# Performance work log

Hardware: AMD Instinct MI355X
Metric: run time of the kernel (lower is better)

The kernel has to match this reference:

```python
import jax, jax.numpy as jnp
import numpy as np

C = 1024
H = 16
D = C // H

def setup_inputs() -> dict:
    key = jax.random.key(0)
    ks = jax.random.split(key, 12)
    s = 1.0 / np.sqrt(C)
    inp = {
        "Q": jax.random.normal(ks[0], (2, 1024, C), jnp.float32),
        "K_in": jax.random.normal(ks[1], (2, 4096, C), jnp.float32),
        "V_in": jax.random.normal(ks[2], (2, 4096, C), jnp.float32),
        "V_bias": jax.random.normal(ks[3], (2, 4096), jnp.float32),
        "Wq_w": jax.random.uniform(ks[4], (C, C), jnp.float32, -s, s),
        "Wq_b": jax.random.uniform(ks[5], (C,), jnp.float32, -s, s),
        "Wk_w": jax.random.uniform(ks[6], (C, C), jnp.float32, -s, s),
        "Wk_b": jax.random.uniform(ks[7], (C,), jnp.float32, -s, s),
        "Wv_w": jax.random.uniform(ks[8], (C, C), jnp.float32, -s, s),
        "Wv_b": jax.random.uniform(ks[9], (C,), jnp.float32, -s, s),
        "Wo_w": jax.random.uniform(ks[10], (C, C), jnp.float32, -s, s),
        "Wo_b": jax.random.uniform(ks[11], (C,), jnp.float32, -s, s),
    }
    return inp

def reference(Q, K_in, V_in, V_bias, Wq_w, Wq_b, Wk_w, Wk_b, Wv_w, Wv_b, Wo_w, Wo_b):
    B, Lq, _ = Q.shape
    Lk = K_in.shape[1]
    # linear projections (torch Linear: x @ W.T + b), split heads -> [B,H,L,D]
    q = (Q @ Wq_w.T + Wq_b).reshape(B, Lq, H, D).transpose(0, 2, 1, 3)
    k = (K_in @ Wk_w.T + Wk_b).reshape(B, Lk, H, D).transpose(0, 2, 1, 3)
    v = (V_in @ Wv_w.T + Wv_b).reshape(B, Lk, H, D).transpose(0, 2, 1, 3)
    scale = 1.0 / np.sqrt(D).astype(np.float32)
    logits = jnp.einsum("bhqd,bhkd->bhqk", q, k) * scale
    logits = logits + V_bias[:, None, None, :]  # per-key additive bias
    attn = jax.nn.softmax(logits, axis=-1)      # dropout p=0.0 (eval)
    out = jnp.einsum("bhqk,bhkd->bhqd", attn, v)
    out = out.transpose(0, 2, 1, 3).reshape(B, Lq, C)
    return out @ Wo_w.T + Wo_b
```

## Files before the change

### kernel.cpp

```cpp
#include <hip/hip_runtime.h>


typedef __attribute__((ext_vector_type(8))) __bf16 bf16x8;
typedef __attribute__((ext_vector_type(4))) float f32x4;
typedef __attribute__((ext_vector_type(16))) float f32x16;

#define LOG2E 1.44269504f
#define MFIX 24.0f

__device__ __forceinline__ unsigned short f2bf(float f) {
  union { float f; unsigned u; } v; v.f = f;
  unsigned r = v.u + 0x7fffu + ((v.u >> 16) & 1u);
  return (unsigned short)(r >> 16);
}
__device__ __forceinline__ unsigned short f2h(float x) {
  _Float16 h = (_Float16)x;
  return __builtin_bit_cast(unsigned short, h);
}
__device__ __forceinline__ float h2f(unsigned short u) {
  return (float)__builtin_bit_cast(_Float16, u);
}

__device__ __forceinline__ f32x4 mfma16(bf16x8 a, bf16x8 b, f32x4 c) {
  return __builtin_amdgcn_mfma_f32_16x16x32_bf16(a, b, c, 0, 0, 0);
}
__device__ __forceinline__ f32x16 mfma32(bf16x8 a, bf16x8 b, f32x16 c) {
  return __builtin_amdgcn_mfma_f32_32x32x16_bf16(a, b, c, 0, 0, 0);
}

__device__ __forceinline__ unsigned pk2(float lo, float hi) {
  unsigned short a = __builtin_bit_cast(unsigned short, (__bf16)lo);
  unsigned short b = __builtin_bit_cast(unsigned short, (__bf16)hi);
  return (unsigned)a | ((unsigned)b << 16);
}

template <typename T>
__device__ __forceinline__ void gload16(const T* g, T* l) {
  __builtin_amdgcn_global_load_lds(
      (const __attribute__((address_space(1))) void*)g,
      (__attribute__((address_space(3))) void*)l, 16, 0, 0);
}

struct Cvt4 {
  const float* src[4];
  unsigned short* dst[4];
};

__global__ __launch_bounds__(256) void cvt4_kernel(Cvt4 a, int n4) {
  const float4* s = (const float4*)a.src[blockIdx.y];
  unsigned short* d = a.dst[blockIdx.y];
  int stride = gridDim.x * blockDim.x;
  for (int i = blockIdx.x * blockDim.x + threadIdx.x; i < n4; i += stride) {
    float4 f = s[i];
    ushort4 u;
    u.x = f2bf(f.x); u.y = f2bf(f.y); u.z = f2bf(f.z); u.w = f2bf(f.w);
    ((ushort4*)d)[i] = u;
  }
}

__global__ __launch_bounds__(256) void prep_kb(const float* __restrict__ Vb,
                                               unsigned* __restrict__ kb) {
  const int i = blockIdx.x * 256 + threadIdx.x;
  const float x = Vb[i] * LOG2E;
  const unsigned short h = f2bf(x);
  union { unsigned u; float f; } hf; hf.u = (unsigned)h << 16;
  const unsigned short lo = f2bf(x - hf.f);
  kb[i] = (unsigned)h | ((unsigned)lo << 16);
}

struct ProjSeg {
  const void* A; const unsigned short* W; const float* bias; void* out;
  int mode; int Llog2; float oscale;
};
struct ProjArgs { ProjSeg s[3]; int start1, start2; };

template <bool AF32>
__global__ __launch_bounds__(256, 2) void proj_gemm(ProjArgs pa) {
  constexpr int K = 1024, N = 1024;
  __shared__ unsigned short Alds[128][40];
  __shared__ unsigned short Blds[2][128][32];

  const int bid = blockIdx.x;
  const int si = (bid >= pa.start1) + (bid >= pa.start2);
  const ProjSeg sg = pa.s[si];
  const int base = si == 0 ? 0 : (si == 1 ? pa.start1 : pa.start2);
  const int local = bid - base;
  const int xcd = local & 7, jj = local >> 3;
  const int m0 = ((jj >> 3) * 8 + xcd) * 128;
  const int n0 = (jj & 7) * 128;

  const int tid = threadIdx.x;
  const int wid = tid >> 6, l = tid & 63;
  const int wr = wid >> 1, wc = wid & 1;
  const int lg = l >> 4, lm = l & 15;

  const int crow = tid >> 2;
  const int ck8 = (tid & 3) * 8;

  const float* Af = (const float*)sg.A;
  const unsigned short* Ab = (const unsigned short*)sg.A;

  const int brow = wid * 16 + (l >> 2);
  const int bcol = ((l & 3) ^ ((l >> 3) & 3)) * 8;
  const unsigned short* bsrc0 = sg.W + (long)(n0 + brow) * K + bcol;
  const unsigned short* bsrc1 = sg.W + (long)(n0 + 64 + brow) * K + bcol;

  f32x4 acc[4][4] = {};
  uint4 ra[2][2];

  auto loadA = [&](int kt) {
#pragma unroll
    for (int half = 0; half < 2; ++half) {
      const long off = (long)(m0 + crow + half * 64) * K + kt * 32 + ck8;
      if constexpr (AF32) {
        ra[half][0] = *(const uint4*)(Af + off);
        ra[half][1] = *(const uint4*)(Af + off + 4);
      } else {
        ra[half][0] = *(const uint4*)(Ab + off);
      }
    }
  };
  auto cvtA = [&](int half) -> uint4 {
    if constexpr (AF32) {
      union { uint4 u[2]; float f[8]; } t;
      t.u[0] = ra[half][0]; t.u[1] = ra[half][1];
      bf16x8 v;
#pragma unroll
      for (int e = 0; e < 8; ++e) v[e] = (__bf16)t.f[e];
      uint4 u; __builtin_memcpy(&u, &v, 16);
      return u;
    } else {
      return ra[half][0];
    }
  };
  auto issueB = [&](int kt, int buf) {
    gload16(bsrc0 + kt * 32, &Blds[buf][wid * 16][0]);
    gload16(bsrc1 + kt * 32, &Blds[buf][64 + wid * 16][0]);
  };

  issueB(0, 0);
  loadA(0);

  for (int kt = 0; kt < K / 32; ++kt) {
    const int buf = kt & 1;
    __syncthreads();
    *(uint4*)&Alds[crow][ck8] = cvtA(0);
    *(uint4*)&Alds[crow + 64][ck8] = cvtA(1);
    __syncthreads();
    if (kt + 1 < K / 32) {
      issueB(kt + 1, buf ^ 1);
      loadA(kt + 1);
    }

    bf16x8 af[4], bfr[4];
#pragma unroll
    for (int i = 0; i < 4; ++i)
      af[i] = *(const bf16x8*)&Alds[wr * 64 + i * 16 + lm][lg * 8];
#pragma unroll
    for (int j = 0; j < 4; ++j)
      bfr[j] = *(const bf16x8*)
          &Blds[buf][wc * 64 + j * 16 + lm][(lg ^ ((lm >> 1) & 3)) * 8];

    __builtin_amdgcn_s_setprio(1);
    if (sg.mode == 1) {
#pragma unroll
      for (int i = 0; i < 4; ++i)
#pragma unroll
        for (int j = 0; j < 4; ++j)
          acc[i][j] = mfma16(bfr[i], af[j], acc[i][j]);
    } else {
#pragma unroll
      for (int i = 0; i < 4; ++i)
#pragma unroll
        for (int j = 0; j < 4; ++j)
          acc[i][j] = mfma16(af[i], bfr[j], acc[i][j]);
    }
    __builtin_amdgcn_s_setprio(0);
  }

  const int rr = lg * 4;
  if (sg.mode == 0) {
    const int Lmask = (1 << sg.Llog2) - 1;
    unsigned short* out = (unsigned short*)sg.out;
#pragma unroll
    for (int j = 0; j < 4; ++j) {
      const int n = n0 + wc * 64 + j * 16 + lm;
      const float bv = sg.bias[n];
      const int h = n >> 6, d = n & 63;
#pragma unroll
      for (int i = 0; i < 4; ++i)
#pragma unroll
        for (int r = 0; r < 4; ++r) {
          const int m = m0 + wr * 64 + i * 16 + rr + r;
          const int b = m >> sg.Llog2, li = m & Lmask;
          const long o = (((long)(b * 16 + h) << sg.Llog2) + li) * 64 + d;
          out[o] = f2bf((acc[i][j][r] + bv) * sg.oscale);
        }
    }
  } else if (sg.mode == 1) {
    unsigned short* out = (unsigned short*)sg.out;
#pragma unroll
    for (int i = 0; i < 4; ++i)
#pragma unroll
      for (int r = 0; r < 4; ++r) {
        const int n = n0 + wc * 64 + i * 16 + rr + r;
        const float bv = sg.bias[n];
        const int h = n >> 6, d = n & 63;
#pragma unroll
        for (int j = 0; j < 4; ++j) {
          const int m = m0 + wr * 64 + j * 16 + lm;
          const int b = m >> 12, lk = m & 4095;
          const long o = ((long)((b * 16 + h) * 64 + d)) * 4096 + lk;
          out[o] = f2bf(acc[i][j][r] + bv);
        }
      }
  } else {
    float* out = (float*)sg.out;
#pragma unroll
    for (int j = 0; j < 4; ++j) {
      const int n = n0 + wc * 64 + j * 16 + lm;
      const float bv = sg.bias[n];
#pragma unroll
      for (int i = 0; i < 4; ++i)
#pragma unroll
        for (int r = 0; r < 4; ++r) {
          const int m = m0 + wr * 64 + i * 16 + rr + r;
          out[(long)m * N + n] = acc[i][j][r] + bv;
        }
    }
  }
}

__global__ __launch_bounds__(256, 2) void attn64(
    const unsigned short* __restrict__ qh, const unsigned short* __restrict__ kh,
    const unsigned short* __restrict__ vT, const unsigned* __restrict__ kb,
    unsigned short* __restrict__ Oh, float* __restrict__ ml) {
  __shared__ unsigned short Klds[2][64][64];
  __shared__ unsigned short Vlds[2][64][64];

  const int tid = threadIdx.x;
  const int wid = tid >> 6, lane = tid & 63;
  const int lq = lane & 31, hi = lane >> 5;
  const int bh = blockIdx.x, qb = blockIdx.y, sp = blockIdx.z;
  const int b = bh >> 4;
  const int qA = qb * 256 + wid * 64 + lq;
  const int kt0 = sp * 16;

  bf16x8 qrA[4], qrB[4];
  {
    const unsigned short* qp = qh + ((long)bh * 1024 + qA) * 64 + hi * 8;
#pragma unroll
    for (int dc = 0; dc < 4; ++dc) {
      qrA[dc] = *(const bf16x8*)(qp + dc * 16);
      qrB[dc] = *(const bf16x8*)(qp + 32 * 64 + dc * 16);
    }
  }

  union uv { uint4 u; bf16x8 v; };
  uv bq; bq.u = make_uint4(hi ? 0u : 0x3F803F80u, 0u, 0u, 0u);

  auto swap23 = [](int r) { return (r & 0x33) | ((r & 4) << 1) | ((r & 8) >> 1); };
  const int r0 = wid * 16 + (lane >> 3), r1 = r0 + 8;
  const int s0 = ((lane & 7) ^ (r0 & 7)) * 8;
  const int s1 = ((lane & 7) ^ (r1 & 7)) * 8;
  const unsigned short* kg0 =
      kh + ((long)bh * 4096 + kt0 * 64 + swap23(r0)) * 64 + s0;
  const unsigned short* kg1 =
      kh + ((long)bh * 4096 + kt0 * 64 + swap23(r1)) * 64 + s1;
  const unsigned short* vg0 = vT + ((long)bh * 64 + r0) * 4096 + kt0 * 64 + s0;
  const unsigned short* vg1 = vT + ((long)bh * 64 + r1) * 4096 + kt0 * 64 + s1;
  const unsigned* kbp = kb + b * 4096 + kt0 * 64;
  const int kbkey = swap23(lq);

  auto issue = [&](int t, int buf) {
    gload16(kg0 + (long)t * 4096, &Klds[buf][wid * 16][0]);
    gload16(kg1 + (long)t * 4096, &Klds[buf][wid * 16 + 8][0]);
    gload16(vg0 + t * 64, &Vlds[buf][wid * 16][0]);
    gload16(vg1 + t * 64, &Vlds[buf][wid * 16 + 8][0]);
  };
  issue(0, 0);

  const int rsw = lq & 7;
  float lA = 0.f, lB = 0.f;
  f32x16 oaA0 = {}, oaA1 = {}, oaB0 = {}, oaB1 = {};
  uv puA[4], puB[4];

  auto softmax = [&](const f32x16& sx0, const f32x16& sx1, float& lreg,
                     uv* pu) {
    float p[32];
#pragma unroll
    for (int r = 0; r < 16; ++r) {
      p[r] = __builtin_amdgcn_exp2f(sx0[r] - MFIX);
      p[16 + r] = __builtin_amdgcn_exp2f(sx1[r] - MFIX);
    }
    float s16[16];
#pragma unroll
    for (int i = 0; i < 16; ++i) s16[i] = p[i] + p[i + 16];
#pragma unroll
    for (int s = 8; s > 0; s >>= 1)
#pragma unroll
      for (int i = 0; i < 8; ++i)
        if (i < s) s16[i] += s16[i + s];
    lreg += s16[0] + __shfl_xor(s16[0], 32);
#pragma unroll
    for (int kc = 0; kc < 4; ++kc)
      pu[kc].u = make_uint4(pk2(p[kc * 8 + 0], p[kc * 8 + 1]),
                            pk2(p[kc * 8 + 2], p[kc * 8 + 3]),
                            pk2(p[kc * 8 + 4], p[kc * 8 + 5]),
                            pk2(p[kc * 8 + 6], p[kc * 8 + 7]));
  };

  for (int t = 0; t < 16; ++t) {
    const int buf = t & 1;
    __syncthreads();
    if (t + 1 < 16) issue(t + 1, buf ^ 1);

    uv ka0, ka1;
    ka0.u = make_uint4(hi ? 0u : kbp[t * 64 + kbkey], 0u, 0u, 0u);
    ka1.u = make_uint4(hi ? 0u : kbp[t * 64 + 32 + kbkey], 0u, 0u, 0u);

    bf16x8 kf0[4], kf1[4];
#pragma unroll
    for (int dc = 0; dc < 4; ++dc) {
      const int so = ((dc * 2 + hi) ^ rsw) * 8;
      kf0[dc] = *(const bf16x8*)&Klds[buf][lq][so];
      kf1[dc] = *(const bf16x8*)&Klds[buf][32 + lq][so];
    }

    f32x16 sa0 = {}, sa1 = {}, sb0 = {}, sb1 = {};
    __builtin_amdgcn_s_setprio(1);
#pragma unroll
    for (int dc = 0; dc < 4; ++dc) {
      sa0 = mfma32(kf0[dc], qrA[dc], sa0);
      sa1 = mfma32(kf1[dc], qrA[dc], sa1);
      sb0 = mfma32(kf0[dc], qrB[dc], sb0);
      sb1 = mfma32(kf1[dc], qrB[dc], sb1);
    }
    sa0 = mfma32(ka0.v, bq.v, sa0);
    sa1 = mfma32(ka1.v, bq.v, sa1);
    sb0 = mfma32(ka0.v, bq.v, sb0);
    sb1 = mfma32(ka1.v, bq.v, sb1);
    __builtin_amdgcn_s_setprio(0);

    softmax(sa0, sa1, lA, puA);

    bf16x8 vf0[4], vf1[4];
#pragma unroll
    for (int kc = 0; kc < 4; ++kc) {
      const int so = ((kc * 2 + hi) ^ rsw) * 8;
      vf0[kc] = *(const bf16x8*)&Vlds[buf][lq][so];
      vf1[kc] = *(const bf16x8*)&Vlds[buf][32 + lq][so];
    }

    __builtin_amdgcn_s_setprio(1);
#pragma unroll
    for (int kc = 0; kc < 4; ++kc) {
      oaA0 = mfma32(vf0[kc], puA[kc].v, oaA0);
      oaA1 = mfma32(vf1[kc], puA[kc].v, oaA1);
    }
    __builtin_amdgcn_s_setprio(0);

    softmax(sb0, sb1, lB, puB);

    __builtin_amdgcn_s_setprio(1);
#pragma unroll
    for (int kc = 0; kc < 4; ++kc) {
      oaB0 = mfma32(vf0[kc], puB[kc].v, oaB0);
      oaB1 = mfma32(vf1[kc], puB[kc].v, oaB1);
    }
    __builtin_amdgcn_s_setprio(0);
  }

  const float invA = 1.0f / lA, invB = 1.0f / lB;
  unsigned short* obA = Oh + (((long)sp * 32 + bh) * 1024 + qA) * 64 + hi * 4;
  unsigned short* obB = obA + 32 * 64;
#pragma unroll
  for (int g = 0; g < 4; ++g) {
    ushort4 u;
    u.x = f2h(oaA0[g * 4 + 0] * invA); u.y = f2h(oaA0[g * 4 + 1] * invA);
    u.z = f2h(oaA0[g * 4 + 2] * invA); u.w = f2h(oaA0[g * 4 + 3] * invA);
    *(ushort4*)(obA + g * 8) = u;
    u.x = f2h(oaA1[g * 4 + 0] * invA); u.y = f2h(oaA1[g * 4 + 1] * invA);
    u.z = f2h(oaA1[g * 4 + 2] * invA); u.w = f2h(oaA1[g * 4 + 3] * invA);
    *(ushort4*)(obA + 32 + g * 8) = u;
    u.x = f2h(oaB0[g * 4 + 0] * invB); u.y = f2h(oaB0[g * 4 + 1] * invB);
    u.z = f2h(oaB0[g * 4 + 2] * invB); u.w = f2h(oaB0[g * 4 + 3] * invB);
    *(ushort4*)(obB + g * 8) = u;
    u.x = f2h(oaB1[g * 4 + 0] * invB); u.y = f2h(oaB1[g * 4 + 1] * invB);
    u.z = f2h(oaB1[g * 4 + 2] * invB); u.w = f2h(oaB1[g * 4 + 3] * invB);
    *(ushort4*)(obB + 32 + g * 8) = u;
  }
  if (hi == 0) {
    *(float2*)(ml + (((long)sp * 32 + bh) * 1024 + qA) * 2) =
        make_float2(MFIX, lA);
    *(float2*)(ml + (((long)sp * 32 + bh) * 1024 + qA + 32) * 2) =
        make_float2(MFIX, lB);
  }
}

__global__ __launch_bounds__(256) void combine4(
    const unsigned short* __restrict__ Oh, const float* __restrict__ ml,
    unsigned short* __restrict__ ao) {
  const int idx = blockIdx.x * 256 + threadIdx.x;
  const int bh = idx >> 10, q = idx & 1023;
  const int b = bh >> 4, h = bh & 15;
  float m[4], l[4];
#pragma unroll
  for (int i = 0; i < 4; ++i) {
    float2 t = *(const float2*)(ml + ((long)i * 32768 + idx) * 2);
    m[i] = t.x; l[i] = t.y;
  }
  const float mm = fmaxf(fmaxf(m[0], m[1]), fmaxf(m[2], m[3]));
  float w[4], wsum = 0.f;
#pragma unroll
  for (int i = 0; i < 4; ++i) {
    w[i] = l[i] * __builtin_amdgcn_exp2f(m[i] - mm);
    wsum += w[i];
  }
  const float inv = 1.0f / wsum;
#pragma unroll
  for (int i = 0; i < 4; ++i) w[i] *= inv;

  unsigned short* op = ao + ((long)b * 1024 + q) * 1024 + h * 64;
#pragma unroll
  for (int blk = 0; blk < 8; ++blk) {
    float acc[8] = {};
#pragma unroll
    for (int i = 0; i < 4; ++i) {
      uint4 u = *(const uint4*)(Oh + ((long)i * 32768 + idx) * 64 + blk * 8);
      const unsigned short* hs = (const unsigned short*)&u;
#pragma unroll
      for (int j = 0; j < 8; ++j) acc[j] += w[i] * h2f(hs[j]);
    }
    ushort4 o0, o1;
    o0.x = f2bf(acc[0]); o0.y = f2bf(acc[1]);
    o0.z = f2bf(acc[2]); o0.w = f2bf(acc[3]);
    o1.x = f2bf(acc[4]); o1.y = f2bf(acc[5]);
    o1.z = f2bf(acc[6]); o1.w = f2bf(acc[7]);
    *(ushort4*)(op + blk * 8) = o0;
    *(ushort4*)(op + blk * 8 + 4) = o1;
  }
}

extern "C" void kernel_launch(void* const* d_in, const int* in_sizes, int n_in,
                              void* d_out, int out_size, void* d_ws,
                              size_t ws_size, hipStream_t stream) {
  const float* Q = (const float*)d_in[0];
  const float* K_in = (const float*)d_in[1];
  const float* V_in = (const float*)d_in[2];
  const float* V_bias = (const float*)d_in[3];
  const float* Wq_w = (const float*)d_in[4];
  const float* Wq_b = (const float*)d_in[5];
  const float* Wk_w = (const float*)d_in[6];
  const float* Wk_b = (const float*)d_in[7];
  const float* Wv_w = (const float*)d_in[8];
  const float* Wv_b = (const float*)d_in[9];
  const float* Wo_w = (const float*)d_in[10];
  const float* Wo_b = (const float*)d_in[11];

  char* ws = (char*)d_ws;
  unsigned short* Wqb = (unsigned short*)(ws + (0l << 20));
  float* mlp = (float*)(ws + (0l << 20));
  unsigned short* Wkb = (unsigned short*)(ws + (2l << 20));
  unsigned short* Wvb = (unsigned short*)(ws + (4l << 20));
  unsigned short* Wob = (unsigned short*)(ws + (6l << 20));
  unsigned short* qhp = (unsigned short*)(ws + (8l << 20));
  unsigned short* khp = (unsigned short*)(ws + (12l << 20));
  unsigned short* vTp = (unsigned short*)(ws + (28l << 20));
  unsigned short* Ohp = (unsigned short*)(ws + (44l << 20));
  unsigned short* aop = (unsigned short*)(ws + (60l << 20));
  unsigned* kbp = (unsigned*)(ws + (64l << 20));

  Cvt4 c4;
  c4.src[0] = Wq_w; c4.src[1] = Wk_w; c4.src[2] = Wv_w; c4.src[3] = Wo_w;
  c4.dst[0] = Wqb;  c4.dst[1] = Wkb;  c4.dst[2] = Wvb;  c4.dst[3] = Wob;
  cvt4_kernel<<<dim3(256, 4), 256, 0, stream>>>(c4, (1024 * 1024) / 4);
  prep_kb<<<32, 256, 0, stream>>>(V_bias, kbp);

  ProjArgs pj;
  pj.s[0] = ProjSeg{K_in, Wkb, Wk_b, khp, 0, 12, 1.0f};
  pj.s[1] = ProjSeg{V_in, Wvb, Wv_b, vTp, 1, 12, 1.0f};
  pj.s[2] = ProjSeg{Q, Wqb, Wq_b, qhp, 0, 10, 0.125f * LOG2E};
  pj.start1 = 512; pj.start2 = 1024;
  proj_gemm<true><<<1152, 256, 0, stream>>>(pj);

  attn64<<<dim3(32, 4, 4), 256, 0, stream>>>(qhp, khp, vTp, kbp, Ohp, mlp);
  combine4<<<128, 256, 0, stream>>>(Ohp, mlp, aop);

  ProjArgs po;
  po.s[0] = ProjSeg{aop, Wob, Wo_b, d_out, 2, 0, 1.0f};
  po.s[1] = po.s[0]; po.s[2] = po.s[0];
  po.start1 = 1 << 30; po.start2 = 1 << 30;
  proj_gemm<false><<<128, 256, 0, stream>>>(po);
}
```

Measured before the change: 200.5 us.

## Pre-convert activations to bf16 and pipeline projection GEMM with async LDS loads

Activations Q, K_in and V_in are converted to bf16 in separate conversion kernels instead of inside the projection GEMM. The GEMM now loads both A and B tiles straight into LDS via global_load_lds, using a 64-wide K tile with XOR swizzling and two buffers issued ahead with vmcnt waits. The K/Q projection and the V projection run as separate launches so the bf16 scratch buffers can share workspace. The aim is to remove per-iteration register conversion and halve the barriers per K step. The cost is extra HBM traffic to write and reread the bf16 activation copies, plus more kernel launches.

```diff
diff --git a/kernel.cpp b/kernel.cpp
--- a/kernel.cpp
+++ b/kernel.cpp
@@ -41,16 +41,15 @@
       (__attribute__((address_space(3))) void*)l, 16, 0, 0);
 }
 
-struct Cvt4 {
-  const float* src[4];
-  unsigned short* dst[4];
-};
-
-__global__ __launch_bounds__(256) void cvt4_kernel(Cvt4 a, int n4) {
-  const float4* s = (const float4*)a.src[blockIdx.y];
-  unsigned short* d = a.dst[blockIdx.y];
-  int stride = gridDim.x * blockDim.x;
-  for (int i = blockIdx.x * blockDim.x + threadIdx.x; i < n4; i += stride) {
+struct CvtJob { const float* src; unsigned short* dst; int n4; };
+struct CvtArgs { CvtJob j[6]; };
+
+__global__ __launch_bounds__(256) void cvt_kernel(CvtArgs a) {
+  const CvtJob jb = a.j[blockIdx.y];
+  const float4* s = (const float4*)jb.src;
+  unsigned short* d = jb.dst;
+  const int stride = gridDim.x * blockDim.x;
+  for (int i = blockIdx.x * blockDim.x + threadIdx.x; i < jb.n4; i += stride) {
     float4 f = s[i];
     ushort4 u;
     u.x = f2bf(f.x); u.y = f2bf(f.y); u.z = f2bf(f.z); u.w = f2bf(f.w);
@@ -69,22 +68,20 @@
 }
 
 struct ProjSeg {
-  const void* A; const unsigned short* W; const float* bias; void* out;
-  int mode; int Llog2; float oscale;
+  const unsigned short* A; const unsigned short* W; const float* bias;
+  void* out; int mode; int Llog2; float oscale;
 };
-struct ProjArgs { ProjSeg s[3]; int start1, start2; };
-
-template <bool AF32>
+struct ProjArgs { ProjSeg s[2]; int start1; };
+
 __global__ __launch_bounds__(256, 2) void proj_gemm(ProjArgs pa) {
-  constexpr int K = 1024, N = 1024;
-  __shared__ unsigned short Alds[128][40];
-  __shared__ unsigned short Blds[2][128][32];
+  constexpr int K = 1024;
+  __shared__ unsigned short Alds[2][128][64];
+  __shared__ unsigned short Blds[2][128][64];
 
   const int bid = blockIdx.x;
-  const int si = (bid >= pa.start1) + (bid >= pa.start2);
+  const int si = (bid >= pa.start1) ? 1 : 0;
   const ProjSeg sg = pa.s[si];
-  const int base = si == 0 ? 0 : (si == 1 ? pa.start1 : pa.start2);
-  const int local = bid - base;
+  const int local = bid - (si ? pa.start1 : 0);
   const int xcd = local & 7, jj = local >> 3;
   const int m0 = ((jj >> 3) * 8 + xcd) * 128;
   const int n0 = (jj & 7) * 128;
@@ -94,88 +91,61 @@
   const int wr = wid >> 1, wc = wid & 1;
   const int lg = l >> 4, lm = l & 15;
 
-  const int crow = tid >> 2;
-  const int ck8 = (tid & 3) * 8;
-
-  const float* Af = (const float*)sg.A;
-  const unsigned short* Ab = (const unsigned short*)sg.A;
-
-  const int brow = wid * 16 + (l >> 2);
-  const int bcol = ((l & 3) ^ ((l >> 3) & 3)) * 8;
-  const unsigned short* bsrc0 = sg.W + (long)(n0 + brow) * K + bcol;
-  const unsigned short* bsrc1 = sg.W + (long)(n0 + 64 + brow) * K + bcol;
+  const int srow = wid * 8 + (l >> 3);
+  const int scol = ((l & 7) ^ (l >> 3)) * 8;
+  const unsigned short* aS = sg.A + (long)(m0 + srow) * K + scol;
+  const unsigned short* bS = sg.W + (long)(n0 + srow) * K + scol;
 
   f32x4 acc[4][4] = {};
-  uint4 ra[2][2];
-
-  auto loadA = [&](int kt) {
-#pragma unroll
-    for (int half = 0; half < 2; ++half) {
-      const long off = (long)(m0 + crow + half * 64) * K + kt * 32 + ck8;
-      if constexpr (AF32) {
-        ra[half][0] = *(const uint4*)(Af + off);
-        ra[half][1] = *(const uint4*)(Af + off + 4);
+
+  auto issue = [&](int kt, int buf) {
+#pragma unroll
+    for (int c = 0; c < 4; ++c) {
+      gload16(aS + ((long)c * 32) * K + kt * 64,
+              &Alds[buf][c * 32 + wid * 8][0]);
+      gload16(bS + ((long)c * 32) * K + kt * 64,
+              &Blds[buf][c * 32 + wid * 8][0]);
+    }
+  };
+
+  issue(0, 0);
+  issue(1, 1);
+
+  for (int t = 0; t < 16; ++t) {
+    if (t < 15) asm volatile("s_waitcnt vmcnt(8)" ::: "memory");
+    else        asm volatile("s_waitcnt vmcnt(0)" ::: "memory");
+    __builtin_amdgcn_sched_barrier(0);
+    __builtin_amdgcn_s_barrier();
+    const int buf = t & 1;
+
+#pragma unroll
+    for (int kc = 0; kc < 2; ++kc) {
+      bf16x8 af[4], bf[4];
+#pragma unroll
+      for (int i = 0; i < 4; ++i) {
+        const int so = ((kc * 4 + lg) ^ (lm & 7)) * 8;
+        af[i] = *(const bf16x8*)&Alds[buf][wr * 64 + i * 16 + lm][so];
+        bf[i] = *(const bf16x8*)&Blds[buf][wc * 64 + i * 16 + lm][so];
+      }
+      __builtin_amdgcn_s_setprio(1);
+      if (sg.mode == 1) {
+#pragma unroll
+        for (int i = 0; i < 4; ++i)
+#pragma unroll
+          for (int j = 0; j < 4; ++j)
+            acc[i][j] = mfma16(bf[i], af[j], acc[i][j]);
       } else {
-        ra[half][0] = *(const uint4*)(Ab + off);
+#pragma unroll
+        for (int i = 0; i < 4; ++i)
+#pragma unroll
+          for (int j = 0; j < 4; ++j)
+            acc[i][j] = mfma16(af[i], bf[j], acc[i][j]);
       }
-    }
-  };
-  auto cvtA = [&](int half) -> uint4 {
-    if constexpr (AF32) {
-      union { uint4 u[2]; float f[8]; } t;
-      t.u[0] = ra[half][0]; t.u[1] = ra[half][1];
-      bf16x8 v;
-#pragma unroll
-      for (int e = 0; e < 8; ++e) v[e] = (__bf16)t.f[e];
-      uint4 u; __builtin_memcpy(&u, &v, 16);
-      return u;
-    } else {
-      return ra[half][0];
-    }
-  };
-  auto issueB = [&](int kt, int buf) {
-    gload16(bsrc0 + kt * 32, &Blds[buf][wid * 16][0]);
-    gload16(bsrc1 + kt * 32, &Blds[buf][64 + wid * 16][0]);
-  };
-
-  issueB(0, 0);
-  loadA(0);
-
-  for (int kt = 0; kt < K / 32; ++kt) {
-    const int buf = kt & 1;
-    __syncthreads();
-    *(uint4*)&Alds[crow][ck8] = cvtA(0);
-    *(uint4*)&Alds[crow + 64][ck8] = cvtA(1);
-    __syncthreads();
-    if (kt + 1 < K / 32) {
-      issueB(kt + 1, buf ^ 1);
-      loadA(kt + 1);
-    }
-
-    bf16x8 af[4], bfr[4];
-#pragma unroll
-    for (int i = 0; i < 4; ++i)
-      af[i] = *(const bf16x8*)&Alds[wr * 64 + i * 16 + lm][lg * 8];
-#pragma unroll
-    for (int j = 0; j < 4; ++j)
-      bfr[j] = *(const bf16x8*)
-          &Blds[buf][wc * 64 + j * 16 + lm][(lg ^ ((lm >> 1) & 3)) * 8];
-
-    __builtin_amdgcn_s_setprio(1);
-    if (sg.mode == 1) {
-#pragma unroll
-      for (int i = 0; i < 4; ++i)
-#pragma unroll
-        for (int j = 0; j < 4; ++j)
-          acc[i][j] = mfma16(bfr[i], af[j], acc[i][j]);
-    } else {
-#pragma unroll
-      for (int i = 0; i < 4; ++i)
-#pragma unroll
-        for (int j = 0; j < 4; ++j)
-          acc[i][j] = mfma16(af[i], bfr[j], acc[i][j]);
-    }
-    __builtin_amdgcn_s_setprio(0);
+      __builtin_amdgcn_s_setprio(0);
+    }
+
+    __builtin_amdgcn_s_barrier();
+    if (t + 2 < 16) issue(t + 2, buf);
   }
 
   const int rr = lg * 4;
@@ -225,7 +195,7 @@
 #pragma unroll
         for (int r = 0; r < 4; ++r) {
           const int m = m0 + wr * 64 + i * 16 + rr + r;
-          out[(long)m * N + n] = acc[i][j][r] + bv;
+          out[(long)m * 1024 + n] = acc[i][j][r] + bv;
         }
     }
   }
@@ -467,29 +437,47 @@
   unsigned short* qhp = (unsigned short*)(ws + (8l << 20));
   unsigned short* khp = (unsigned short*)(ws + (12l << 20));
   unsigned short* vTp = (unsigned short*)(ws + (28l << 20));
+  unsigned short* Qbf = (unsigned short*)(ws + (44l << 20));
+  unsigned short* Kbf = (unsigned short*)(ws + (48l << 20));
+  unsigned short* Vbf = (unsigned short*)(ws + (48l << 20));
   unsigned short* Ohp = (unsigned short*)(ws + (44l << 20));
   unsigned short* aop = (unsigned short*)(ws + (60l << 20));
   unsigned* kbp = (unsigned*)(ws + (64l << 20));
 
-  Cvt4 c4;
-  c4.src[0] = Wq_w; c4.src[1] = Wk_w; c4.src[2] = Wv_w; c4.src[3] = Wo_w;
-  c4.dst[0] = Wqb;  c4.dst[1] = Wkb;  c4.dst[2] = Wvb;  c4.dst[3] = Wob;
-  cvt4_kernel<<<dim3(256, 4), 256, 0, stream>>>(c4, (1024 * 1024) / 4);
+  CvtArgs c1;
+  c1.j[0] = CvtJob{Wq_w, Wqb, 262144};
+  c1.j[1] = CvtJob{Wk_w, Wkb, 262144};
+  c1.j[2] = CvtJob{Wv_w, Wvb, 262144};
+  c1.j[3] = CvtJob{Wo_w, Wob, 262144};
+  c1.j[4] = CvtJob{Q, Qbf, 524288};
+  c1.j[5] = CvtJob{K_in, Kbf, 2097152};
+  cvt_kernel<<<dim3(512, 6), 256, 0, stream>>>(c1);
   prep_kb<<<32, 256, 0, stream>>>(V_bias, kbp);
 
-  ProjArgs pj;
-  pj.s[0] = ProjSeg{K_in, Wkb, Wk_b, khp, 0, 12, 1.0f};
-  pj.s[1] = ProjSeg{V_in, Wvb, Wv_b, vTp, 1, 12, 1.0f};
-  pj.s[2] = ProjSeg{Q, Wqb, Wq_b, qhp, 0, 10, 0.125f * LOG2E};
-  pj.start1 = 512; pj.start2 = 1024;
-  proj_gemm<true><<<1152, 256, 0, stream>>>(pj);
+  ProjArgs pA;
+  pA.s[0] = ProjSeg{Kbf, Wkb, Wk_b, khp, 0, 12, 1.0f};
+  pA.s[1] = ProjSeg{Qbf, Wqb, Wq_b, qhp, 0, 10, 0.125f * LOG2E};
+  pA.start1 = 512;
+  proj_gemm<<<640, 256, 0, stream>>>(pA);
+
+  CvtArgs c2;
+  c2.j[0] = CvtJob{V_in, Vbf, 2097152};
+  c2.j[1] = c2.j[0]; c2.j[2] = c2.j[0];
+  c2.j[3] = c2.j[0]; c2.j[4] = c2.j[0]; c2.j[5] = c2.j[0];
+  cvt_kernel<<<dim3(512, 1), 256, 0, stream>>>(c2);
+
+  ProjArgs pB;
+  pB.s[0] = ProjSeg{Vbf, Wvb, Wv_b, vTp, 1, 12, 1.0f};
+  pB.s[1] = pB.s[0];
+  pB.start1 = 1 << 30;
+  proj_gemm<<<512, 256, 0, stream>>>(pB);
 
   attn64<<<dim3(32, 4, 4), 256, 0, stream>>>(qhp, khp, vTp, kbp, Ohp, mlp);
   combine4<<<128, 256, 0, stream>>>(Ohp, mlp, aop);
 
-  ProjArgs po;
-  po.s[0] = ProjSeg{aop, Wob, Wo_b, d_out, 2, 0, 1.0f};
-  po.s[1] = po.s[0]; po.s[2] = po.s[0];
-  po.start1 = 1 << 30; po.start2 = 1 << 30;
-  proj_gemm<false><<<128, 256, 0, stream>>>(po);
-}
+  ProjArgs pO;
+  pO.s[0] = ProjSeg{aop, Wob, Wo_b, d_out, 2, 0, 1.0f};
+  pO.s[1] = pO.s[0];
+  pO.start1 = 1 << 30;
+  proj_gemm<<<128, 256, 0, stream>>>(pO);
+}
```

Result: faster. 172.0 us (-14.2%).
